# Performance work log

Hardware: AMD Instinct MI355X
Metric: run time of the kernel (lower is better)

## Reference

```python
import jax, jax.numpy as jnp
import numpy as np

N, B, L, E = 64, 128, 4096, 16
BN_EPS = 1e-5


def setup_inputs() -> dict:
    key = jax.random.key(0)
    ks = jax.random.split(key, 6)
    feat = jax.random.normal(ks[0], (N, B, L), dtype=jnp.float32)
    # Glorot-ish scaled linear weights
    Wl = jax.random.normal(ks[1], (L, E), dtype=jnp.float32) * (1.0 / np.sqrt(L))
    Wr = jax.random.normal(ks[2], (L, E), dtype=jnp.float32) * (1.0 / np.sqrt(L))
    Wm = jax.random.normal(ks[3], (L, L), dtype=jnp.float32) * (1.0 / np.sqrt(L))
    return {
        "feat": feat,
        "Wl": Wl, "bl": jnp.zeros((E,), jnp.float32),
        "Wr": Wr, "br": jnp.zeros((E,), jnp.float32),
        "Wm": Wm, "bm": jnp.zeros((L,), jnp.float32),
        "gamma": jnp.ones((N * N,), jnp.float32),
        "beta": jnp.zeros((N * N,), jnp.float32),
        "bias": jnp.zeros((L,), jnp.float32),
    }


def reference(feat, Wl, bl, Wr, br, Wm, bm, gamma, beta, bias):
    # feat: (N, B, L) node time series
    # Attention projections (lookup_l / lookup_r): Linear(L -> E)
    att_l = feat @ Wl + bl                      # (N, B, E) on src nodes
    att_r = feat @ Wr + br                      # (N, B, E) on dst nodes

    # Feature extractor: MLP Linear(L, L) + ReLU over the time axis
    out = jax.nn.relu(jnp.einsum('nbl,kl->nbk', feat, Wm) + bm)   # (N, B, L)

    # Edge scores on the complete graph: e[d, s, b] = att_l[src=s] . att_r[dst=d]
    e = jnp.einsum('sbe,dbe->dsb', att_l, att_r)                  # (Nd, Ns, B)

    # BatchNorm1d over N*N edge channels (training-mode batch statistics)
    ef = e.reshape(N * N, B)
    mu = ef.mean(axis=1, keepdims=True)
    var = ef.var(axis=1, keepdims=True)
    ef = gamma[:, None] * (ef - mu) * jax.lax.rsqrt(var + BN_EPS) + beta[:, None]
    e = ef.reshape(N, N, B)

    # edge_softmax: normalize over incoming edges (src axis) per destination node
    w = jax.nn.softmax(e, axis=1)                                  # (Nd, Ns, B)

    # Weighted neighbor aggregation + bias
    rst = jnp.einsum('dsb,sbl->dbl', w, out) + bias                # (N, B, L)
    return rst
```

## Files before the change

### kernel.cpp

```cpp
#include <hip/hip_runtime.h>
#include <stdint.h>
#include <stddef.h>

#define NN 64
#define BB 128
#define LL 4096
#define EE 16

typedef __attribute__((ext_vector_type(4))) float f32x4;
typedef __attribute__((ext_vector_type(2))) float f32x2;
typedef __attribute__((ext_vector_type(8))) short short8;
typedef __attribute__((ext_vector_type(4))) unsigned short u16x4;

__device__ __forceinline__ unsigned short f2bf(float f) {
  union { float f; unsigned u; } v; v.f = f;
  unsigned r = v.u + 0x7FFFu + ((v.u >> 16) & 1u);
  return (unsigned short)(r >> 16);
}
__device__ __forceinline__ float bf2f(unsigned short h) {
  union { unsigned u; float f; } v; v.u = ((unsigned)h) << 16;
  return v.f;
}
__device__ __forceinline__ void gload16(const void* g, void* l) {
  __builtin_amdgcn_global_load_lds((const __attribute__((address_space(1))) void*)g,
                                   (__attribute__((address_space(3))) void*)l,
                                   16, 0, 0);
}

#define MFMA(a, b, c) __builtin_amdgcn_mfma_f32_16x16x32_bf16((a), (b), (c), 0, 0, 0)

__global__ __launch_bounds__(256) void k_cvtw(const float* __restrict__ Wm,
    const float* __restrict__ Wl, const float* __restrict__ Wr,
    unsigned short* __restrict__ wm_bf, unsigned short* __restrict__ wt_bf) {
  int bid = blockIdx.x;
  if (bid < 2048) {
    int i = bid * 256 + threadIdx.x;
    for (; i < (LL * LL / 4); i += 2048 * 256) {
      f32x4 v = ((const f32x4*)Wm)[i];
      u16x4 o;
      o[0] = f2bf(v[0]); o[1] = f2bf(v[1]); o[2] = f2bf(v[2]); o[3] = f2bf(v[3]);
      ((u16x4*)wm_bf)[i] = o;
    }
  } else {
    int u = (bid - 2048) * 256 + threadIdx.x;
    int e = u >> 6;
    int kb = (u & 63) * 64;
    const float* src = (e < 16) ? (Wl + e) : (Wr + (e - 16));
    for (int k = kb; k < kb + 64; ++k)
      wt_bf[(size_t)e * LL + k] = f2bf(src[(size_t)k * 16]);
  }
}

__global__ __launch_bounds__(256) void k_attF(const float* __restrict__ feat,
    const unsigned short* __restrict__ wt_bf,
    unsigned short* __restrict__ feat_bf, float* __restrict__ attP) {
  __shared__ __align__(16) unsigned short alds[64 * 512];
  const int t = threadIdx.x, lane = t & 63, w = t >> 6;
  const int rowBase = blockIdx.x * 64;
  const int kBase = blockIdx.y * 2048;
  const int rr = lane & 15, gg8 = (lane >> 4) * 8;
  f32x4 acc0 = {}, acc1 = {};
  const unsigned short* b0P = wt_bf + (size_t)rr * LL;
  const unsigned short* b1P = wt_bf + (size_t)(16 + rr) * LL;
  for (int c = 0; c < 4; ++c) {
    const int k0 = kBase + c * 512;
    __syncthreads();
    #pragma unroll
    for (int u = 0; u < 32; ++u) {
      int unit = t + u * 256;
      int row = unit >> 7, col4 = unit & 127;
      size_t gi = (size_t)(rowBase + row) * LL + k0 + col4 * 4;
      f32x4 v = *(const f32x4*)&feat[gi];
      u16x4 o; o[0] = f2bf(v[0]); o[1] = f2bf(v[1]); o[2] = f2bf(v[2]); o[3] = f2bf(v[3]);
      *(u16x4*)&feat_bf[gi] = o;
      int byte = (row * 1024 + col4 * 8) ^ ((row & 7) << 4);
      *(u16x4*)((char*)alds + byte) = o;
    }
    __syncthreads();
    const int arow = w * 16 + rr;
    const char* aBase = (const char*)alds + arow * 1024;
    const int axor = (arow & 7) << 4;
    #pragma unroll 4
    for (int ks = 0; ks < 16; ++ks) {
      int abyte = ((ks * 32 + gg8) * 2) ^ axor;
      short8 av = *(const short8*)(aBase + abyte);
      short8 b0 = *(const short8*)(b0P + k0 + ks * 32 + gg8);
      short8 b1 = *(const short8*)(b1P + k0 + ks * 32 + gg8);
      acc0 = MFMA(av, b0, acc0);
      acc1 = MFMA(av, b1, acc1);
    }
  }
  const int orow = rowBase + w * 16 + (lane >> 4) * 4;
  float* P = attP + (size_t)blockIdx.y * (8192 * 32);
  #pragma unroll
  for (int j = 0; j < 4; ++j) {
    P[(size_t)(orow + j) * 32 + rr]      = acc0[j];
    P[(size_t)(orow + j) * 32 + 16 + rr] = acc1[j];
  }
}

__global__ __launch_bounds__(256) void k_edge(const float* __restrict__ attP,
    const float* __restrict__ bl, const float* __restrict__ br,
    const float* __restrict__ gamma, const float* __restrict__ beta,
    float* __restrict__ w_t) {
  __shared__ __align__(16) float attr[BB][20];
  __shared__ float el[NN][BB + 1];
  __shared__ float part[NN][4][2];
  __shared__ float sc[NN], sh[NN];
  int d = blockIdx.x, t = threadIdx.x;
  for (int i = t; i < 2048; i += 256) {
    int b = i >> 4, e = i & 15;
    float v2 = br[e];
    #pragma unroll
    for (int c = 0; c < 2; ++c)
      v2 += attP[(size_t)c * (8192 * 32) + ((size_t)d * 128 + b) * 32 + 16 + e];
    attr[b][e] = v2;
  }
  float blv[16];
  #pragma unroll
  for (int e = 0; e < 16; ++e) blv[e] = bl[e];
  __syncthreads();
  for (int v = t; v < NN * BB; v += 256) {
    int s = v >> 7, b = v & 127;
    float al[16];
    #pragma unroll
    for (int e = 0; e < 16; ++e) al[e] = blv[e];
    #pragma unroll
    for (int c = 0; c < 2; ++c) {
      const f32x4* p = (const f32x4*)&attP[(size_t)c * (8192 * 32) + ((size_t)s * 128 + b) * 32];
      #pragma unroll
      for (int q = 0; q < 4; ++q) {
        f32x4 x = p[q];
        al[q * 4 + 0] += x[0]; al[q * 4 + 1] += x[1];
        al[q * 4 + 2] += x[2]; al[q * 4 + 3] += x[3];
      }
    }
    float acc = 0.f;
    #pragma unroll
    for (int e = 0; e < 16; ++e) acc += al[e] * attr[b][e];
    el[s][b] = acc;
  }
  __syncthreads();
  {
    int s = t >> 2, q = t & 3;
    float sum = 0.f, ss = 0.f;
    for (int b = q * 32; b < q * 32 + 32; ++b) { float x = el[s][b]; sum += x; ss += x * x; }
    part[s][q][0] = sum; part[s][q][1] = ss;
  }
  __syncthreads();
  if (t < 64) {
    float sum = 0.f, ss = 0.f;
    #pragma unroll
    for (int q = 0; q < 4; ++q) { sum += part[t][q][0]; ss += part[t][q][1]; }
    float mu = sum * (1.f / 128.f);
    float var = ss * (1.f / 128.f) - mu * mu;
    int c = d * 64 + t;
    float a = gamma[c] * rsqrtf(fmaxf(var, 0.f) + 1e-5f);
    sc[t] = a; sh[t] = beta[c] - mu * a;
  }
  __syncthreads();
  if (t < 128) {
    int b = t;
    float y[64];
    float m = -1e30f;
    #pragma unroll
    for (int s = 0; s < 64; ++s) { y[s] = sc[s] * el[s][b] + sh[s]; m = fmaxf(m, y[s]); }
    float sum = 0.f;
    #pragma unroll
    for (int s = 0; s < 64; ++s) { y[s] = __expf(y[s] - m); sum += y[s]; }
    float inv = 1.f / sum;
    float* wp = &w_t[((size_t)b * 64 + d) * 64];
    #pragma unroll
    for (int s4 = 0; s4 < 16; ++s4) {
      f32x4 o;
      o[0] = y[s4 * 4 + 0] * inv; o[1] = y[s4 * 4 + 1] * inv;
      o[2] = y[s4 * 4 + 2] * inv; o[3] = y[s4 * 4 + 3] * inv;
      *(f32x4*)&wp[s4 * 4] = o;
    }
  }
}

#define BAR   __builtin_amdgcn_s_barrier()
#define VM6   asm volatile("s_waitcnt vmcnt(6)" ::: "memory")
#define VM0   asm volatile("s_waitcnt vmcnt(0)" ::: "memory")
#define NOVM  do {} while (0)
#define PRIO1 __builtin_amdgcn_s_setprio(1)
#define PRIO0 __builtin_amdgcn_s_setprio(0)

#define STAGE6(STG, KK) do { \
    gload16(aG0 + (KK),            ldsm + (STG) * 8192 + tid16); \
    gload16(aG0 + 64 * LL + (KK),  ldsm + (STG) * 8192 + 4096 + tid16); \
    gload16(bG0 + (KK),            ldsm + 24576 + (STG) * 16384 + tid16); \
    gload16(bG0 + 64 * LL + (KK),  ldsm + 24576 + (STG) * 16384 + 4096 + tid16); \
    gload16(bG0 + 128 * LL + (KK), ldsm + 24576 + (STG) * 16384 + 8192 + tid16); \
    gload16(bG0 + 192 * LL + (KK), ldsm + 24576 + (STG) * 16384 + 12288 + tid16); \
  } while (0)

#define GITER(T, CUR, STG, DOSTAGE, VMW) do { \
    const char* pA = ldsm + (CUR) * 8192 + wm * 4096 + rdswz; \
    const char* pB = ldsm + 24576 + (CUR) * 16384 + wn * 8192 + rdswz; \
    short8 af[4], bf[8]; \
    _Pragma("unroll") for (int mi = 0; mi < 4; ++mi) af[mi] = *(const short8*)(pA + mi * 1024); \
    _Pragma("unroll") for (int nj = 0; nj < 8; ++nj) bf[nj] = *(const short8*)(pB + nj * 1024); \
    if (DOSTAGE) { STAGE6(STG, (size_t)((T) + 2) * 32); } \
    PRIO1; \
    _Pragma("unroll") for (int mi = 0; mi < 4; ++mi) \
      _Pragma("unroll") for (int nj = 0; nj < 8; ++nj) \
        acc[mi][nj] = MFMA(af[mi], bf[nj], acc[mi][nj]); \
    PRIO0; VMW; BAR; \
  } while (0)

__global__ __launch_bounds__(256, 2) void k_gemmW(const unsigned short* __restrict__ A,
    const unsigned short* __restrict__ Bm, const float* __restrict__ bm,
    unsigned short* __restrict__ C) {
  __shared__ __align__(16) char ldsm[73728];
  const int tid = threadIdx.x;
  const int lane = tid & 63, wave = tid >> 6;
  const int wm = wave >> 1, wn = wave & 1;
  int bid = blockIdx.x;
  int swz = (bid & 7) * 128 + (bid >> 3);
  int tM = swz >> 4, tN = swz & 15;
  const size_t rowBase = (size_t)tM * 128, colBase = (size_t)tN * 256;
  const int tid16 = tid * 16;
  const int srow = tid >> 2;
  const int qx = (tid & 3) ^ (((tid >> 5) & 1) << 1);
  const unsigned short* aG0 = A  + (rowBase + srow) * LL + qx * 8;
  const unsigned short* bG0 = Bm + (colBase + srow) * LL + qx * 8;
  const int rr = lane & 15, gg = lane >> 4;
  const int rdswz = rr * 64 + ((gg ^ ((rr >> 3) << 1)) << 4);
  f32x4 acc[4][8] = {};
  STAGE6(0, 0);
  STAGE6(1, 32);
  VM6;
  BAR;
  for (int tb = 0; tb < 126; tb += 3) {
    GITER(tb,     0, 2, 1, VM6);
    GITER(tb + 1, 1, 0, 1, VM6);
    GITER(tb + 2, 2, 1, 1, VM6);
  }
  GITER(126, 0, 0, 0, VM0);
  GITER(127, 1, 0, 0, NOVM);
  const int co = lane & 15, ro4 = (lane >> 4) * 4;
  #pragma unroll
  for (int mig = 0; mig < 4; ++mig) {
    size_t r0 = rowBase + (size_t)wm * 64 + mig * 16 + ro4;
    #pragma unroll
    for (int nj = 0; nj < 8; ++nj) {
      size_t c = colBase + (size_t)wn * 128 + nj * 16 + co;
      float bc = bm[c];
      #pragma unroll
      for (int j = 0; j < 4; ++j) {
        float v = acc[mig][nj][j] + bc;
        v = fmaxf(v, 0.f);
        C[(r0 + j) * LL + c] = f2bf(v);
      }
    }
  }
}

__global__ __launch_bounds__(256) void k_agg2(const float* __restrict__ w_t,
    const unsigned short* __restrict__ outb, const float* __restrict__ bias,
    float* __restrict__ rst) {
  int b = blockIdx.y;
  int t = threadIdx.x;
  int l0 = blockIdx.x * 512 + t * 2;
  float oA[64], oB[64];
  #pragma unroll
  for (int s = 0; s < 64; ++s) {
    unsigned u = *(const unsigned*)&outb[((size_t)s * BB + b) * LL + l0];
    oA[s] = bf2f((unsigned short)(u & 0xFFFF));
    oB[s] = bf2f((unsigned short)(u >> 16));
  }
  const float* wb = w_t + (size_t)b * 4096;
  float bs0 = bias[l0], bs1 = bias[l0 + 1];
  #pragma unroll 2
  for (int d = 0; d < 64; ++d) {
    const float* wr = wb + d * 64;
    float a0 = 0.f, a1 = 0.f;
    #pragma unroll
    for (int q = 0; q < 16; ++q) {
      f32x4 wq = *(const f32x4*)&wr[q * 4];
      #pragma unroll
      for (int j = 0; j < 4; ++j) {
        float wv = wq[j];
        a0 += wv * oA[q * 4 + j];
        a1 += wv * oB[q * 4 + j];
      }
    }
    f32x2 o; o[0] = a0 + bs0; o[1] = a1 + bs1;
    *(f32x2*)&rst[((size_t)d * BB + b) * LL + l0] = o;
  }
}

extern "C" void kernel_launch(void* const* d_in, const int* in_sizes, int n_in,
                              void* d_out, int out_size, void* d_ws, size_t ws_size,
                              hipStream_t stream) {
  (void)in_sizes; (void)n_in; (void)out_size; (void)ws_size;
  const float* feat  = (const float*)d_in[0];
  const float* Wl    = (const float*)d_in[1];
  const float* bl    = (const float*)d_in[2];
  const float* Wr    = (const float*)d_in[3];
  const float* br    = (const float*)d_in[4];
  const float* Wm    = (const float*)d_in[5];
  const float* bm    = (const float*)d_in[6];
  const float* gamma = (const float*)d_in[7];
  const float* beta  = (const float*)d_in[8];
  const float* bias  = (const float*)d_in[9];
  char* ws = (char*)d_ws;
  unsigned short* feat_bf = (unsigned short*)(ws);
  unsigned short* wm_bf   = (unsigned short*)(ws + 67108864ull);
  unsigned short* out_bf  = (unsigned short*)(ws + 100663296ull);
  float* attP  = (float*)(ws + 167772160ull);
  float* w_t   = (float*)(ws + 169869312ull);
  unsigned short* wt_bf = (unsigned short*)(ws + 171966464ull);
  float* rst = (float*)d_out;

  k_cvtw<<<dim3(2056), dim3(256), 0, stream>>>(Wm, Wl, Wr, wm_bf, wt_bf);
  k_attF<<<dim3(128, 2), dim3(256), 0, stream>>>(feat, wt_bf, feat_bf, attP);
  k_edge<<<dim3(64), dim3(256), 0, stream>>>(attP, bl, br, gamma, beta, w_t);
  k_gemmW<<<dim3(1024), dim3(256), 0, stream>>>(feat_bf, wm_bf, bm, out_bf);
  k_agg2<<<dim3(8, 128), dim3(256), 0, stream>>>(w_t, out_bf, bias, rst);
}
```

Baseline: 466.2 us.

## Switch main GEMM to 256x256 tiles with 32x32x16 bf16 MFMA

Rewrites the big feat×Wm GEMM to use 256x256 block tiles, with each wave computing 128x128 through 32x32x16 bf16 MFMAs, in place of 128x256 tiles built from 16x16x32 MFMAs. The larger tile raises arithmetic intensity and reuse of the LDS operands. It also cuts the number of LDS fragment reads per MFMA and halves the block count to 512. The cost is 96KB of LDS and a much larger accumulator, which limits occupancy to one block per CU. The grid shrinks to 512 blocks, which raises the risk of tail imbalance across the CUs.

Measured after the change: 463.1 us. About the same (-0.7%).

```diff
diff --git a/kernel.cpp b/kernel.cpp
--- a/kernel.cpp
+++ b/kernel.cpp
@@ -8,6 +8,7 @@
 #define EE 16
 
 typedef __attribute__((ext_vector_type(4))) float f32x4;
+typedef __attribute__((ext_vector_type(16))) float f32x16;
 typedef __attribute__((ext_vector_type(2))) float f32x2;
 typedef __attribute__((ext_vector_type(8))) short short8;
 typedef __attribute__((ext_vector_type(4))) unsigned short u16x4;
@@ -27,7 +28,8 @@
                                    16, 0, 0);
 }
 
-#define MFMA(a, b, c) __builtin_amdgcn_mfma_f32_16x16x32_bf16((a), (b), (c), 0, 0, 0)
+#define MFMA(a, b, c)   __builtin_amdgcn_mfma_f32_16x16x32_bf16((a), (b), (c), 0, 0, 0)
+#define MFMA32(a, b, c) __builtin_amdgcn_mfma_f32_32x32x16_bf16((a), (b), (c), 0, 0, 0)
 
 __global__ __launch_bounds__(256) void k_cvtw(const float* __restrict__ Wm,
     const float* __restrict__ Wl, const float* __restrict__ Wr,
@@ -181,78 +183,89 @@
 }
 
 #define BAR   __builtin_amdgcn_s_barrier()
-#define VM6   asm volatile("s_waitcnt vmcnt(6)" ::: "memory")
+#define VM8   asm volatile("s_waitcnt vmcnt(8)" ::: "memory")
 #define VM0   asm volatile("s_waitcnt vmcnt(0)" ::: "memory")
 #define NOVM  do {} while (0)
 #define PRIO1 __builtin_amdgcn_s_setprio(1)
 #define PRIO0 __builtin_amdgcn_s_setprio(0)
 
-#define STAGE6(STG, KK) do { \
-    gload16(aG0 + (KK),            ldsm + (STG) * 8192 + tid16); \
-    gload16(aG0 + 64 * LL + (KK),  ldsm + (STG) * 8192 + 4096 + tid16); \
-    gload16(bG0 + (KK),            ldsm + 24576 + (STG) * 16384 + tid16); \
-    gload16(bG0 + 64 * LL + (KK),  ldsm + 24576 + (STG) * 16384 + 4096 + tid16); \
-    gload16(bG0 + 128 * LL + (KK), ldsm + 24576 + (STG) * 16384 + 8192 + tid16); \
-    gload16(bG0 + 192 * LL + (KK), ldsm + 24576 + (STG) * 16384 + 12288 + tid16); \
+#define STAGE8(STG, KK) do { \
+    _Pragma("unroll") for (int i_ = 0; i_ < 4; ++i_) \
+      gload16(aGs + (size_t)i_ * 64 * LL + (KK), ldsm + (STG) * 32768 + i_ * 4096 + tid16); \
+    _Pragma("unroll") for (int i_ = 0; i_ < 4; ++i_) \
+      gload16(bGs + (size_t)i_ * 64 * LL + (KK), ldsm + (STG) * 32768 + 16384 + i_ * 4096 + tid16); \
   } while (0)
 
-#define GITER(T, CUR, STG, DOSTAGE, VMW) do { \
-    const char* pA = ldsm + (CUR) * 8192 + wm * 4096 + rdswz; \
-    const char* pB = ldsm + 24576 + (CUR) * 16384 + wn * 8192 + rdswz; \
-    short8 af[4], bf[8]; \
-    _Pragma("unroll") for (int mi = 0; mi < 4; ++mi) af[mi] = *(const short8*)(pA + mi * 1024); \
-    _Pragma("unroll") for (int nj = 0; nj < 8; ++nj) bf[nj] = *(const short8*)(pB + nj * 1024); \
-    if (DOSTAGE) { STAGE6(STG, (size_t)((T) + 2) * 32); } \
+#define GITER32(T, CUR, STG, DOSTAGE, VMW) do { \
+    const char* pA = ldsm + (CUR) * 32768 + baseA; \
+    const char* pB = ldsm + (CUR) * 32768 + baseB; \
+    short8 af[4], bf[4]; \
+    _Pragma("unroll") for (int mi = 0; mi < 4; ++mi) af[mi] = *(const short8*)(pA + mi * 2048 + offK0); \
+    _Pragma("unroll") for (int nj = 0; nj < 4; ++nj) bf[nj] = *(const short8*)(pB + nj * 2048 + offK0); \
+    if (DOSTAGE) { STAGE8(STG, (size_t)((T) + 2) * 32); } \
     PRIO1; \
     _Pragma("unroll") for (int mi = 0; mi < 4; ++mi) \
-      _Pragma("unroll") for (int nj = 0; nj < 8; ++nj) \
-        acc[mi][nj] = MFMA(af[mi], bf[nj], acc[mi][nj]); \
+      _Pragma("unroll") for (int nj = 0; nj < 4; ++nj) \
+        acc[mi][nj] = MFMA32(af[mi], bf[nj], acc[mi][nj]); \
+    PRIO0; \
+    _Pragma("unroll") for (int mi = 0; mi < 4; ++mi) af[mi] = *(const short8*)(pA + mi * 2048 + offK1); \
+    _Pragma("unroll") for (int nj = 0; nj < 4; ++nj) bf[nj] = *(const short8*)(pB + nj * 2048 + offK1); \
+    PRIO1; \
+    _Pragma("unroll") for (int mi = 0; mi < 4; ++mi) \
+      _Pragma("unroll") for (int nj = 0; nj < 4; ++nj) \
+        acc[mi][nj] = MFMA32(af[mi], bf[nj], acc[mi][nj]); \
     PRIO0; VMW; BAR; \
   } while (0)
 
-__global__ __launch_bounds__(256, 2) void k_gemmW(const unsigned short* __restrict__ A,
+__global__ __launch_bounds__(256, 1) void k_gemm32(const unsigned short* __restrict__ A,
     const unsigned short* __restrict__ Bm, const float* __restrict__ bm,
     unsigned short* __restrict__ C) {
-  __shared__ __align__(16) char ldsm[73728];
+  __shared__ __align__(16) char ldsm[98304];
   const int tid = threadIdx.x;
   const int lane = tid & 63, wave = tid >> 6;
   const int wm = wave >> 1, wn = wave & 1;
   int bid = blockIdx.x;
-  int swz = (bid & 7) * 128 + (bid >> 3);
+  int swz = (bid & 7) * 64 + (bid >> 3);
   int tM = swz >> 4, tN = swz & 15;
-  const size_t rowBase = (size_t)tM * 128, colBase = (size_t)tN * 256;
+  const size_t rowBase = (size_t)tM * 256, colBase = (size_t)tN * 256;
   const int tid16 = tid * 16;
   const int srow = tid >> 2;
-  const int qx = (tid & 3) ^ (((tid >> 5) & 1) << 1);
-  const unsigned short* aG0 = A  + (rowBase + srow) * LL + qx * 8;
-  const unsigned short* bG0 = Bm + (colBase + srow) * LL + qx * 8;
-  const int rr = lane & 15, gg = lane >> 4;
-  const int rdswz = rr * 64 + ((gg ^ ((rr >> 3) << 1)) << 4);
-  f32x4 acc[4][8] = {};
-  STAGE6(0, 0);
-  STAGE6(1, 32);
-  VM6;
+  const int sslot = (tid & 3) ^ ((tid >> 3) & 3);
+  const unsigned short* aGs = A  + (rowBase + srow) * LL + sslot * 8;
+  const unsigned short* bGs = Bm + (colBase + srow) * LL + sslot * 8;
+  const int lrow = lane & 31, lhw = lane >> 5, lw = (lane >> 1) & 3;
+  const int baseA = (wm * 128 + lrow) * 64;
+  const int baseB = 16384 + (wn * 128 + lrow) * 64;
+  const int offK0 = ((lhw) ^ lw) * 16;
+  const int offK1 = ((2 + lhw) ^ lw) * 16;
+  f32x16 acc[4][4] = {};
+  STAGE8(0, 0);
+  STAGE8(1, 32);
+  VM8;
   BAR;
   for (int tb = 0; tb < 126; tb += 3) {
-    GITER(tb,     0, 2, 1, VM6);
-    GITER(tb + 1, 1, 0, 1, VM6);
-    GITER(tb + 2, 2, 1, 1, VM6);
-  }
-  GITER(126, 0, 0, 0, VM0);
-  GITER(127, 1, 0, 0, NOVM);
-  const int co = lane & 15, ro4 = (lane >> 4) * 4;
-  #pragma unroll
-  for (int mig = 0; mig < 4; ++mig) {
-    size_t r0 = rowBase + (size_t)wm * 64 + mig * 16 + ro4;
-    #pragma unroll
-    for (int nj = 0; nj < 8; ++nj) {
-      size_t c = colBase + (size_t)wn * 128 + nj * 16 + co;
-      float bc = bm[c];
+    GITER32(tb,     0, 2, 1, VM8);
+    GITER32(tb + 1, 1, 0, 1, VM8);
+    GITER32(tb + 2, 2, 1, 1, VM8);
+  }
+  GITER32(126, 0, 0, 0, VM0);
+  GITER32(127, 1, 0, 0, NOVM);
+  const int cl = lane & 31, rh = (lane >> 5) * 4;
+  float bcv[4];
+  #pragma unroll
+  for (int nj = 0; nj < 4; ++nj) bcv[nj] = bm[colBase + wn * 128 + nj * 32 + cl];
+  #pragma unroll
+  for (int mi = 0; mi < 4; ++mi) {
+    #pragma unroll
+    for (int nj = 0; nj < 4; ++nj) {
+      size_t c = colBase + (size_t)wn * 128 + nj * 32 + cl;
+      float bc = bcv[nj];
       #pragma unroll
-      for (int j = 0; j < 4; ++j) {
-        float v = acc[mig][nj][j] + bc;
+      for (int r = 0; r < 16; ++r) {
+        size_t row = rowBase + (size_t)wm * 128 + mi * 32 + (r & 3) + 8 * (r >> 2) + rh;
+        float v = acc[mi][nj][r] + bc;
         v = fmaxf(v, 0.f);
-        C[(r0 + j) * LL + c] = f2bf(v);
+        C[row * LL + c] = f2bf(v);
       }
     }
   }
@@ -318,6 +331,6 @@
   k_cvtw<<<dim3(2056), dim3(256), 0, stream>>>(Wm, Wl, Wr, wm_bf, wt_bf);
   k_attF<<<dim3(128, 2), dim3(256), 0, stream>>>(feat, wt_bf, feat_bf, attP);
   k_edge<<<dim3(64), dim3(256), 0, stream>>>(attP, bl, br, gamma, beta, w_t);
-  k_gemmW<<<dim3(1024), dim3(256), 0, stream>>>(feat_bf, wm_bf, bm, out_bf);
+  k_gemm32<<<dim3(512), dim3(256), 0, stream>>>(feat_bf, wm_bf, bm, out_bf);
   k_agg2<<<dim3(8, 128), dim3(256), 0, stream>>>(w_t, out_bf, bias, rst);
 }
```

## Enlarge GEMM tile to 256x256 with 8 waves, 4-stage LDS pipeline

Applied to the files above, without the earlier changes.

Replaces the 128x256 tile, 4-wave GEMM with a 256x256 tile computed by 8 waves in 512-thread blocks. The K loop now uses a 4-stage LDS ring with 3 tiles prefetched, and A fragments are double-buffered in registers so the next tile's A reads overlap the current MFMAs. The aim is higher arithmetic intensity per byte loaded and more latency hiding. In exchange it uses 128KB of LDS, more registers, and half as many blocks, which risks lower occupancy and tail imbalance.

Result: slower. 507.0 us (+8.7%).

```diff
diff --git a/kernel.cpp b/kernel.cpp
--- a/kernel.cpp
+++ b/kernel.cpp
@@ -181,72 +181,91 @@
 }
 
 #define BAR   __builtin_amdgcn_s_barrier()
-#define VM6   asm volatile("s_waitcnt vmcnt(6)" ::: "memory")
+#define VM4   asm volatile("s_waitcnt vmcnt(4)" ::: "memory")
 #define VM0   asm volatile("s_waitcnt vmcnt(0)" ::: "memory")
 #define NOVM  do {} while (0)
 #define PRIO1 __builtin_amdgcn_s_setprio(1)
 #define PRIO0 __builtin_amdgcn_s_setprio(0)
 
-#define STAGE6(STG, KK) do { \
-    gload16(aG0 + (KK),            ldsm + (STG) * 8192 + tid16); \
-    gload16(aG0 + 64 * LL + (KK),  ldsm + (STG) * 8192 + 4096 + tid16); \
-    gload16(bG0 + (KK),            ldsm + 24576 + (STG) * 16384 + tid16); \
-    gload16(bG0 + 64 * LL + (KK),  ldsm + 24576 + (STG) * 16384 + 4096 + tid16); \
-    gload16(bG0 + 128 * LL + (KK), ldsm + 24576 + (STG) * 16384 + 8192 + tid16); \
-    gload16(bG0 + 192 * LL + (KK), ldsm + 24576 + (STG) * 16384 + 12288 + tid16); \
+#define STAGEP(S, TT) do { \
+    size_t kk = (size_t)(TT) * 32; \
+    gload16(aR0 + kk, ldsm + (S) * 16384 + tid16); \
+    gload16(aR1 + kk, ldsm + (S) * 16384 + 8192 + tid16); \
+    gload16(bR0 + kk, ldsm + 65536 + (S) * 16384 + tid16); \
+    gload16(bR1 + kk, ldsm + 65536 + (S) * 16384 + 8192 + tid16); \
   } while (0)
 
-#define GITER(T, CUR, STG, DOSTAGE, VMW) do { \
-    const char* pA = ldsm + (CUR) * 8192 + wm * 4096 + rdswz; \
-    const char* pB = ldsm + 24576 + (CUR) * 16384 + wn * 8192 + rdswz; \
-    short8 af[4], bf[8]; \
-    _Pragma("unroll") for (int mi = 0; mi < 4; ++mi) af[mi] = *(const short8*)(pA + mi * 1024); \
-    _Pragma("unroll") for (int nj = 0; nj < 8; ++nj) bf[nj] = *(const short8*)(pB + nj * 1024); \
-    if (DOSTAGE) { STAGE6(STG, (size_t)((T) + 2) * 32); } \
+#define GITERP(TT, SB, SAN, SST, FC, FN, DONEXT, DOSTAGE, VMW) do { \
+    const char* pB = ldsm + 65536 + (SB) * 16384 + wn * 4096 + rdswz; \
+    short8 bq[4]; \
+    _Pragma("unroll") for (int nj = 0; nj < 4; ++nj) bq[nj] = *(const short8*)(pB + nj * 1024); \
+    if (DONEXT) { \
+      const char* pAn = ldsm + (SAN) * 16384 + wm * 8192 + rdswz; \
+      _Pragma("unroll") for (int mi = 0; mi < 8; ++mi) FN[mi] = *(const short8*)(pAn + mi * 1024); \
+    } \
+    if (DOSTAGE) { STAGEP(SST, (TT) + 3); } \
     PRIO1; \
-    _Pragma("unroll") for (int mi = 0; mi < 4; ++mi) \
-      _Pragma("unroll") for (int nj = 0; nj < 8; ++nj) \
-        acc[mi][nj] = MFMA(af[mi], bf[nj], acc[mi][nj]); \
+    _Pragma("unroll") for (int mi = 0; mi < 8; ++mi) { \
+      acc[mi][0] = MFMA(FC[mi], bq[0], acc[mi][0]); \
+      acc[mi][1] = MFMA(FC[mi], bq[1], acc[mi][1]); \
+      acc[mi][2] = MFMA(FC[mi], bq[2], acc[mi][2]); \
+      acc[mi][3] = MFMA(FC[mi], bq[3], acc[mi][3]); \
+    } \
     PRIO0; VMW; BAR; \
   } while (0)
 
-__global__ __launch_bounds__(256, 2) void k_gemmW(const unsigned short* __restrict__ A,
+__global__ __launch_bounds__(512, 2) void k_gemmP(const unsigned short* __restrict__ A,
     const unsigned short* __restrict__ Bm, const float* __restrict__ bm,
     unsigned short* __restrict__ C) {
-  __shared__ __align__(16) char ldsm[73728];
+  __shared__ __align__(16) char ldsm[131072];
   const int tid = threadIdx.x;
   const int lane = tid & 63, wave = tid >> 6;
-  const int wm = wave >> 1, wn = wave & 1;
+  const int wm = wave >> 2, wn = wave & 3;
   int bid = blockIdx.x;
-  int swz = (bid & 7) * 128 + (bid >> 3);
+  int swz = (bid & 7) * 64 + (bid >> 3);
   int tM = swz >> 4, tN = swz & 15;
-  const size_t rowBase = (size_t)tM * 128, colBase = (size_t)tN * 256;
+  const size_t rowBase = (size_t)tM * 256, colBase = (size_t)tN * 256;
   const int tid16 = tid * 16;
-  const int srow = tid >> 2;
-  const int qx = (tid & 3) ^ (((tid >> 5) & 1) << 1);
-  const unsigned short* aG0 = A  + (rowBase + srow) * LL + qx * 8;
-  const unsigned short* bG0 = Bm + (colBase + srow) * LL + qx * 8;
+  const int o0 = tid16, o1 = tid16 + 8192;
+  const int r0s = (o0 & 1023) >> 6, r1s = (o1 & 1023) >> 6;
+  const int row0 = (o0 >> 10) * 16 + r0s, row1 = (o1 >> 10) * 16 + r1s;
+  const int col0 = (((o0 >> 4) & 3) ^ ((r0s >> 3) << 1)) * 8;
+  const int col1 = (((o1 >> 4) & 3) ^ ((r1s >> 3) << 1)) * 8;
+  const unsigned short* aR0 = A  + (rowBase + row0) * LL + col0;
+  const unsigned short* aR1 = A  + (rowBase + row1) * LL + col1;
+  const unsigned short* bR0 = Bm + (colBase + row0) * LL + col0;
+  const unsigned short* bR1 = Bm + (colBase + row1) * LL + col1;
   const int rr = lane & 15, gg = lane >> 4;
   const int rdswz = rr * 64 + ((gg ^ ((rr >> 3) << 1)) << 4);
-  f32x4 acc[4][8] = {};
-  STAGE6(0, 0);
-  STAGE6(1, 32);
-  VM6;
+  f32x4 acc[8][4] = {};
+  short8 FA[8], FB[8];
+  STAGEP(0, 0);
+  STAGEP(1, 1);
+  STAGEP(2, 2);
+  VM4;
   BAR;
-  for (int tb = 0; tb < 126; tb += 3) {
-    GITER(tb,     0, 2, 1, VM6);
-    GITER(tb + 1, 1, 0, 1, VM6);
-    GITER(tb + 2, 2, 1, 1, VM6);
-  }
-  GITER(126, 0, 0, 0, VM0);
-  GITER(127, 1, 0, 0, NOVM);
+  {
+    const char* pA0 = ldsm + 0 * 16384 + wm * 8192 + rdswz;
+    #pragma unroll
+    for (int mi = 0; mi < 8; ++mi) FA[mi] = *(const short8*)(pA0 + mi * 1024);
+  }
+  for (int tb = 0; tb < 124; tb += 4) {
+    GITERP(tb + 0, 0, 1, 3, FA, FB, 1, 1, VM4);
+    GITERP(tb + 1, 1, 2, 0, FB, FA, 1, 1, VM4);
+    GITERP(tb + 2, 2, 3, 1, FA, FB, 1, 1, VM4);
+    GITERP(tb + 3, 3, 0, 2, FB, FA, 1, 1, VM4);
+  }
+  GITERP(124, 0, 1, 3, FA, FB, 1, 1, VM4);
+  GITERP(125, 1, 2, 0, FB, FA, 1, 0, VM0);
+  GITERP(126, 2, 3, 0, FA, FB, 1, 0, NOVM);
+  GITERP(127, 3, 0, 0, FB, FA, 0, 0, NOVM);
   const int co = lane & 15, ro4 = (lane >> 4) * 4;
   #pragma unroll
-  for (int mig = 0; mig < 4; ++mig) {
-    size_t r0 = rowBase + (size_t)wm * 64 + mig * 16 + ro4;
-    #pragma unroll
-    for (int nj = 0; nj < 8; ++nj) {
-      size_t c = colBase + (size_t)wn * 128 + nj * 16 + co;
+  for (int mig = 0; mig < 8; ++mig) {
+    size_t r0 = rowBase + (size_t)wm * 128 + mig * 16 + ro4;
+    #pragma unroll
+    for (int nj = 0; nj < 4; ++nj) {
+      size_t c = colBase + (size_t)wn * 64 + nj * 16 + co;
       float bc = bm[c];
       #pragma unroll
       for (int j = 0; j < 4; ++j) {
@@ -318,6 +337,6 @@
   k_cvtw<<<dim3(2056), dim3(256), 0, stream>>>(Wm, Wl, Wr, wm_bf, wt_bf);
   k_attF<<<dim3(128, 2), dim3(256), 0, stream>>>(feat, wt_bf, feat_bf, attP);
   k_edge<<<dim3(64), dim3(256), 0, stream>>>(attP, bl, br, gamma, beta, w_t);
-  k_gemmW<<<dim3(1024), dim3(256), 0, stream>>>(feat_bf, wm_bf, bm, out_bf);
+  k_gemmP<<<dim3(512), dim3(512), 0, stream>>>(feat_bf, wm_bf, bm, out_bf);
   k_agg2<<<dim3(8, 128), dim3(256), 0, stream>>>(w_t, out_bf, bias, rst);
 }
```
